# Kernel optimization log

Hardware: AMD Instinct MI355X
Metric: run time of the kernel (lower is better)

## Reference

```python
import jax, jax.numpy as jnp
import numpy as np

EPS = 1e-5

def _ln(x, g, b):
    mu = jnp.mean(x, -1, keepdims=True)
    var = jnp.mean((x - mu) ** 2, -1, keepdims=True)
    return (x - mu) / jnp.sqrt(var + EPS) * g + b

def _edge_scores(x, lat, mask, sn_g, sn_b, tn_g, tn_b, su_w, su_b, tp_w, tp_b, m1_w, m1_b, m2_w, m2_b):
    # x: [B,S,D], lat: [B,K,D] -> edges [B,S,K]
    s = _ln(x, sn_g, sn_b) @ su_w + su_b      # [B,S,E]
    t = _ln(lat, tn_g, tn_b) @ tp_w + tp_b    # [B,K,E]
    B, S, E = s.shape
    K = t.shape[1]
    s4 = jnp.broadcast_to(s[:, :, None, :], (B, S, K, E))
    t4 = jnp.broadcast_to(t[:, None, :, :], (B, S, K, E))
    pair = jnp.concatenate([s4, t4, s4 * t4], axis=-1)  # [B,S,K,3E]
    h = jax.nn.gelu(pair @ m1_w + m1_b, approximate=False)
    e = (h @ m2_w + m2_b)[..., 0]             # [B,S,K]
    e = e / (1.0 + jnp.abs(e))                # softsign
    return e * mask[:, :, None]

def setup_inputs() -> dict:
    key = jax.random.key(0)
    B, St, Si, K, D, E = 2, 2048, 1024, 64, 768, 256
    ks = iter(jax.random.split(key, 64))
    d = {}
    d['text_values'] = jax.random.normal(next(ks), (B, St, D), jnp.float32)
    d['image_values'] = jax.random.normal(next(ks), (B, Si, D), jnp.float32)
    d['latent_state_init'] = jax.random.normal(next(ks), (B, K, D), jnp.float32)
    d['latent_value_init'] = jax.random.normal(next(ks), (B, K, D), jnp.float32)
    d['text_mask'] = jnp.ones((B, St), jnp.float32)
    d['image_mask'] = jnp.ones((B, Si), jnp.float32)
    def scorer(prefix):
        d[prefix + 'sn_g'] = jnp.ones((D,), jnp.float32)
        d[prefix + 'sn_b'] = jnp.zeros((D,), jnp.float32)
        d[prefix + 'tn_g'] = jnp.ones((D,), jnp.float32)
        d[prefix + 'tn_b'] = jnp.zeros((D,), jnp.float32)
        d[prefix + 'su_w'] = jax.random.normal(next(ks), (D, E), jnp.float32) * 0.02
        d[prefix + 'su_b'] = jnp.zeros((E,), jnp.float32)
        d[prefix + 'tp_w'] = jax.random.normal(next(ks), (D, E), jnp.float32) * 0.02
        d[prefix + 'tp_b'] = jnp.zeros((E,), jnp.float32)
        d[prefix + 'm1_w'] = jax.random.normal(next(ks), (3 * E, E), jnp.float32) * 0.02
        d[prefix + 'm1_b'] = jnp.zeros((E,), jnp.float32)
        d[prefix + 'm2_w'] = jax.random.normal(next(ks), (E, 1), jnp.float32) * 0.02
        d[prefix + 'm2_b'] = jnp.zeros((1,), jnp.float32)
    scorer('t_')
    scorer('i_')
    for p in ['tsn', 'isn', 'stn', 'vn']:
        d[p + '_g'] = jnp.ones((D,), jnp.float32)
        d[p + '_b'] = jnp.zeros((D,), jnp.float32)
    d['tsp_w'] = jax.random.normal(next(ks), (D, D), jnp.float32) * 0.02
    d['tsp_b'] = jnp.zeros((D,), jnp.float32)
    d['isp_w'] = jax.random.normal(next(ks), (D, D), jnp.float32) * 0.02
    d['isp_b'] = jnp.zeros((D,), jnp.float32)
    return d

def reference(text_values, image_values, latent_state_init, latent_value_init, text_mask, image_mask,
              t_sn_g, t_sn_b, t_tn_g, t_tn_b, t_su_w, t_su_b, t_tp_w, t_tp_b, t_m1_w, t_m1_b, t_m2_w, t_m2_b,
              i_sn_g, i_sn_b, i_tn_g, i_tn_b, i_su_w, i_su_b, i_tp_w, i_tp_b, i_m1_w, i_m1_b, i_m2_w, i_m2_b,
              tsn_g, tsn_b, isn_g, isn_b, stn_g, stn_b, vn_g, vn_b, tsp_w, tsp_b, isp_w, isp_b):
    t2l = _edge_scores(text_values, latent_value_init, text_mask,
                       t_sn_g, t_sn_b, t_tn_g, t_tn_b, t_su_w, t_su_b, t_tp_w, t_tp_b, t_m1_w, t_m1_b, t_m2_w, t_m2_b)
    i2l = _edge_scores(image_values, latent_value_init, image_mask,
                       i_sn_g, i_sn_b, i_tn_g, i_tn_b, i_su_w, i_su_b, i_tp_w, i_tp_b, i_m1_w, i_m1_b, i_m2_w, i_m2_b)
    tsf = _ln(text_values, tsn_g, tsn_b) @ tsp_w + tsp_b    # [B,St,D]
    isf = _ln(image_values, isn_g, isn_b) @ isp_w + isp_b   # [B,Si,D]
    state_raw = jnp.einsum('bsk,bsd->bkd', t2l, tsf) + jnp.einsum('bsk,bsd->bkd', i2l, isf)
    value_raw = jnp.einsum('bsk,bsd->bkd', t2l, text_values) + jnp.einsum('bsk,bsd->bkd', i2l, image_values)
    latent_state = _ln(state_raw + latent_state_init, stn_g, stn_b)
    latent_value = _ln(value_raw + latent_value_init, vn_g, vn_b)
    return latent_state, latent_value, t2l, i2l
```

## Files before the change

kernel.cpp:

```cpp
#include <hip/hip_runtime.h>
#include <math.h>

#define EPS_LN 1e-5f

#define B_  2
#define ST_ 2048
#define SI_ 1024
#define K_  64
#define D_  768
#define E_  256

typedef __bf16 bf16x8 __attribute__((ext_vector_type(8)));
typedef float  f32x4  __attribute__((ext_vector_type(4)));
typedef unsigned short ushort_t;

__device__ inline ushort_t f2bf(float x) {
    unsigned int u = __float_as_uint(x);
    unsigned int r = (u + 0x7FFFu + ((u >> 16) & 1u)) >> 16;
    return (ushort_t)r;
}

__device__ inline float gelu_fast(float z) {
    float a = fabsf(z);
    float t = __expf(a * -1.702f);
    float r = __builtin_amdgcn_rcpf(1.0f + t);
    float th = fmaf(t * r, -2.0f, 1.0f);
    return fmaf(0.5f * a, th, 0.5f * z);
}


__device__ void ln_stats_body(int bid, int tid,
    const float* __restrict__ xt, const float* __restrict__ xi,
    const float* __restrict__ xl, float* __restrict__ mu, float* __restrict__ rstd)
{
    int w = tid >> 6, lane = tid & 63;
    int row = bid * 4 + w;
    const float* src;
    if (row < 4096) src = xt + (size_t)row * D_;
    else if (row < 6144) src = xi + (size_t)(row - 4096) * D_;
    else src = xl + (size_t)(row - 6144) * D_;
    float s = 0.f, q = 0.f;
    #pragma unroll
    for (int rep = 0; rep < 3; ++rep) {
        float4 v = *(const float4*)(src + lane * 4 + rep * 256);
        s += v.x + v.y + v.z + v.w;
        q += v.x * v.x + v.y * v.y + v.z * v.z + v.w * v.w;
    }
    #pragma unroll
    for (int off = 32; off > 0; off >>= 1) {
        s += __shfl_xor(s, off, 64);
        q += __shfl_xor(q, off, 64);
    }
    if (lane == 0) {
        float m = s / (float)D_;
        float var = q / (float)D_ - m * m;
        mu[row] = m;
        rstd[row] = rsqrtf(var + EPS_LN);
    }
}

__device__ void sgemm_body(char* smem, int tid,
    const float* __restrict__ A, const float* __restrict__ Bm,
    const float* __restrict__ rowScale, const float* __restrict__ bias,
    const float* __restrict__ muA, const float* __restrict__ sdA, int so,
    float* __restrict__ C, int kz, int bx, int by, int Kd, int N)
{
    float (*As)[65] = (float(*)[65])smem;
    float (*Bs)[64] = (float(*)[64])(smem + 16 * 65 * 4);
    int tx = tid & 15, ty = tid >> 4;
    int row0 = by * 64;
    int col0 = bx * 64;
    float acc[4][4] = {};
    int kbase = kz * 128;
    for (int k0 = kbase; k0 < kbase + 128; k0 += 16) {
        {
            int e = tid * 4;
            int r = e >> 4, kk = e & 15;
            float4 av = *(const float4*)(A + (size_t)(row0 + r) * Kd + k0 + kk);
            if (muA) {
                float m = muA[so + row0 + r], sd = sdA[so + row0 + r];
                av.x = (av.x - m) * sd; av.y = (av.y - m) * sd;
                av.z = (av.z - m) * sd; av.w = (av.w - m) * sd;
            }
            As[kk + 0][r] = av.x; As[kk + 1][r] = av.y; As[kk + 2][r] = av.z; As[kk + 3][r] = av.w;
        }
        {
            int e = tid * 4;
            int kk = e >> 6, c = e & 63;
            float4 bv = *(const float4*)(Bm + (size_t)(k0 + kk) * N + col0 + c);
            if (rowScale) {
                float sc = rowScale[k0 + kk];
                bv.x *= sc; bv.y *= sc; bv.z *= sc; bv.w *= sc;
            }
            *(float4*)&Bs[kk][c] = bv;
        }
        __syncthreads();
        #pragma unroll
        for (int kk = 0; kk < 16; ++kk) {
            float a[4], b[4];
            #pragma unroll
            for (int i = 0; i < 4; ++i) a[i] = As[kk][ty + 16 * i];
            #pragma unroll
            for (int j = 0; j < 4; ++j) b[j] = Bs[kk][tx + 16 * j];
            #pragma unroll
            for (int i = 0; i < 4; ++i)
                #pragma unroll
                for (int j = 0; j < 4; ++j)
                    acc[i][j] += a[i] * b[j];
        }
        __syncthreads();
    }
    #pragma unroll
    for (int i = 0; i < 4; ++i) {
        int r = row0 + ty + 16 * i;
        #pragma unroll
        for (int j = 0; j < 4; ++j) {
            int c = col0 + tx + 16 * j;
            float v = acc[i][j];
            if (kz == 0 && bias) v += bias[c];
            atomicAdd(&C[(size_t)r * N + c], v);
        }
    }
}

__global__ __launch_bounds__(256) void prelude_kernel(
    const float* __restrict__ xt, const float* __restrict__ xi,
    const float* __restrict__ xl, float* __restrict__ mu, float* __restrict__ rstd,
    const float* b0, const float* W0, const float* w0, float* f0,
    const float* b1, const float* W1, const float* w1, float* f1,
    const float* b2, const float* W2, const float* w2, float* f2,
    const float* b3, const float* W3, const float* w3, float* f3,
    const float* b4, const float* W4, const float* w4, float* f4,
    const float* b5, const float* W5, const float* w5, float* f5,
    const float* __restrict__ Wsu_t, const float* __restrict__ g_t, ushort_t* __restrict__ WF_t,
    const float* __restrict__ Wsu_i, const float* __restrict__ g_i, ushort_t* __restrict__ WF_i)
{
    extern __shared__ __align__(16) char smem[];
    int bid = blockIdx.x;
    int tid = threadIdx.x;
    if (bid < 1568) {
        ln_stats_body(bid, tid, xt, xi, xl, mu, rstd);
        return;
    }
    if (bid < 2432) {
        int f = bid - 1568;
        int ebx = f % 12, dby = (f / 12) % 12, cfg = f / 144;
        const float* blns[6] = {b0, b1, b2, b3, b4, b5};
        const float* Ws[6]   = {W0, W1, W2, W3, W4, W5};
        const float* wbs[6]  = {w0, w1, w2, w3, w4, w5};
        float* bfs[6]        = {f0, f1, f2, f3, f4, f5};
        int E = (cfg >= 4) ? 768 : 256;
        if (ebx * 64 >= E) return;
        const float* bln = blns[cfg];
        const float* W = Ws[cfg];
        float (*red)[64] = (float(*)[64])smem;
        int c = tid & 63, part = tid >> 6;
        int e = ebx * 64 + c;
        int d0 = dby * 64;
        float s = 0.f;
        #pragma unroll
        for (int i = 0; i < 16; ++i) {
            int d = d0 + part * 16 + i;
            s += bln[d] * W[(size_t)d * E + e];
        }
        red[part][c] = s; __syncthreads();
        if (part == 0) {
            float v = red[0][c] + red[1][c] + red[2][c] + red[3][c];
            if (dby == 0 && wbs[cfg]) v += wbs[cfg][e];
            atomicAdd(&bfs[cfg][e], v);
        }
        return;
    }
    {
        const int HALF = (D_ >> 5) * (E_ >> 4) * 64;
        int gidx = (bid - 2432) * 256 + tid;
        int isImg = gidx >= HALF;
        int idx = isImg ? gidx - HALF : gidx;
        const float* W = isImg ? Wsu_i : Wsu_t;
        const float* g = isImg ? g_i : g_t;
        ushort_t* out = isImg ? WF_i : WF_t;
        int lane = idx & 63;
        int ntile = (idx >> 6) & 15;
        int c = idx >> 10;
        int n = ntile * 16 + (lane & 15);
        int k0 = c * 32 + (lane >> 4) * 8;
        ushort_t o[8];
        #pragma unroll
        for (int j = 0; j < 8; ++j) {
            int k = k0 + j;
            o[j] = f2bf(W[(size_t)k * E_ + n] * g[k]);
        }
        *reinterpret_cast<uint4*>(out + (size_t)idx * 8) = *reinterpret_cast<uint4*>(o);
    }
}

__global__ __launch_bounds__(256) void stage2_kernel(
    const float* __restrict__ xt, const float* __restrict__ xi,
    const float* __restrict__ mu, const float* __restrict__ rstd,
    ushort_t* __restrict__ XrF_t, ushort_t* __restrict__ XhF_t, ushort_t* __restrict__ AF_t,
    ushort_t* __restrict__ XrF_i, ushort_t* __restrict__ XhF_i, ushort_t* __restrict__ AF_i,
    const float* __restrict__ lat,
    const float* __restrict__ t_tp_w, const float* __restrict__ t_tn_g,
    const float* __restrict__ b_tp_t, float* __restrict__ t_t,
    const float* __restrict__ i_tp_w, const float* __restrict__ i_tn_g,
    const float* __restrict__ b_tp_i, float* __restrict__ t_i)
{
    extern __shared__ __align__(16) char smem[];
    int bid = blockIdx.x;
    int t = threadIdx.x;
    if (bid < 1152) {
        int bx = bid % 96, by = bid / 96;
        float (*tile)[65] = (float(*)[65])smem;
        float* mu_s = (float*)(smem + 64 * 65 * 4);
        float* rs_s = mu_s + 64;
        int isImg = bx >= 64;
        const float* x = isImg ? xi : xt;
        ushort_t* XrF = isImg ? XrF_i : XrF_t;
        ushort_t* XhF = isImg ? XhF_i : XhF_t;
        ushort_t* AF  = isImg ? AF_i  : AF_t;
        int rbase = (isImg ? bx - 64 : bx) * 64;
        int statOff = isImg ? 4096 : 0;
        int d0 = by * 64;
        #pragma unroll
        for (int rep = 0; rep < 4; ++rep) {
            int rl = (t >> 4) + rep * 16;
            int c4 = (t & 15) * 4;
            *(float4*)&tile[rl][c4] = *(const float4*)(x + (size_t)(rbase + rl) * D_ + d0 + c4);
        }
        if (t < 64) { mu_s[t] = mu[statOff + rbase + t]; rs_s[t] = rstd[statOff + rbase + t]; }
        __syncthreads();
        int lane = t & 63;
        #pragma unroll
        for (int rep = 0; rep < 2; ++rep) {
            int idx = t + rep * 256;
            int nt = (idx >> 6) & 3, cl = (idx >> 8) & 1;
            int kl = cl * 32 + (lane >> 4) * 8;
            int nl = nt * 16 + (lane & 15);
            ushort_t orw[8], oh[8];
            #pragma unroll
            for (int j = 0; j < 8; ++j) {
                float v = tile[kl + j][nl];
                orw[j] = f2bf(v);
                oh[j]  = f2bf((v - mu_s[kl + j]) * rs_s[kl + j]);
            }
            size_t chunk = (size_t)((rbase >> 5) + cl);
            size_t o = ((chunk * 48 + (d0 >> 4) + nt) * 64 + lane) * 8;
            *reinterpret_cast<uint4*>(XrF + o) = *reinterpret_cast<uint4*>(orw);
            *reinterpret_cast<uint4*>(XhF + o) = *reinterpret_cast<uint4*>(oh);
        }
        #pragma unroll
        for (int rep = 0; rep < 2; ++rep) {
            int idx = t + rep * 256;
            int cl = (idx >> 6) & 1, tl = idx >> 7;
            int rl = tl * 16 + (lane & 15);
            int dl = cl * 32 + (lane >> 4) * 8;
            float m = mu_s[rl], rs = rs_s[rl];
            ushort_t o8[8];
            #pragma unroll
            for (int j = 0; j < 8; ++j)
                o8[j] = f2bf((tile[rl][dl + j] - m) * rs);
            size_t o = (((size_t)(rbase >> 4) + tl) * 24 + (d0 >> 5) + cl) * 512 + lane * 8;
            *reinterpret_cast<uint4*>(AF + o) = *reinterpret_cast<uint4*>(o8);
        }
        return;
    }
    {
        int f = bid - 1152;
        int bx = f % 4, by = (f / 4) % 2, z = f / 8;
        int cfg = (z >= 6) ? 1 : 0;
        int kz = cfg ? z - 6 : z;
        sgemm_body(smem, t,
                   lat, cfg ? i_tp_w : t_tp_w, cfg ? i_tn_g : t_tn_g,
                   cfg ? b_tp_i : b_tp_t, mu, rstd, 6144,
                   cfg ? t_i : t_t, kz, bx, by, D_, E_);
    }
}

__global__ __launch_bounds__(256) void stage3_kernel(
    const float* __restrict__ t_t, const float* __restrict__ t_i,
    const float* __restrict__ t_m1_w, const float* __restrict__ t_m1_b,
    const float* __restrict__ i_m1_w, const float* __restrict__ i_m1_b,
    float* __restrict__ c2_t, float* __restrict__ c2_i,
    const ushort_t* __restrict__ AF_t, const ushort_t* __restrict__ BF_t,
    const float* __restrict__ b_su_t, ushort_t* __restrict__ sF_t,
    const ushort_t* __restrict__ AF_i, const ushort_t* __restrict__ BF_i,
    const float* __restrict__ b_su_i, ushort_t* __restrict__ sF_i,
    ushort_t* __restrict__ MF_t, ushort_t* __restrict__ MF_i)
{
    extern __shared__ __align__(16) char smem[];
    int bid = blockIdx.x;
    int tid = threadIdx.x;
    if (bid < 32) {
        int bx = bid % 4, by = (bid / 4) % 2, z = bid / 8;
        int cfg = (z >= 2) ? 1 : 0;
        int kz = cfg ? z - 2 : z;
        sgemm_body(smem, tid,
                   cfg ? t_i : t_t,
                   (cfg ? i_m1_w : t_m1_w) + (size_t)E_ * E_, nullptr,
                   cfg ? i_m1_b : t_m1_b, nullptr, nullptr, 0,
                   cfg ? c2_i : c2_t, kz, bx, by, E_, E_);
        return;
    }
    if (bid < 224) {
        int bx = bid - 32;
        int isImg = bx >= 128;
        const ushort_t* AF = isImg ? AF_i : AF_t;
        const ushort_t* BF = isImg ? BF_i : BF_t;
        const float* bias = isImg ? b_su_i : b_su_t;
        ushort_t* sF = isImg ? sF_i : sF_t;
        int tile0 = (isImg ? bx - 128 : bx) * 2;
        ushort_t* lsbase = (ushort_t*)smem;
        int w = tid >> 6, lane = tid & 63;
        int quad = lane >> 4, n16 = lane & 15;
        f32x4 acc[2][4];
        #pragma unroll
        for (int mt = 0; mt < 2; ++mt)
            #pragma unroll
            for (int nt = 0; nt < 4; ++nt)
                acc[mt][nt] = (f32x4){0.f, 0.f, 0.f, 0.f};
        for (int c = 0; c < 24; ++c) {
            bf16x8 af[2], bf[4];
            #pragma unroll
            for (int mt = 0; mt < 2; ++mt)
                af[mt] = *reinterpret_cast<const bf16x8*>(AF + ((size_t)(tile0 + mt) * 24 + c) * 512 + lane * 8);
            #pragma unroll
            for (int nt = 0; nt < 4; ++nt)
                bf[nt] = *reinterpret_cast<const bf16x8*>(BF + ((size_t)c * 16 + w * 4 + nt) * 512 + lane * 8);
            #pragma unroll
            for (int mt = 0; mt < 2; ++mt)
                #pragma unroll
                for (int nt = 0; nt < 4; ++nt)
                    acc[mt][nt] = __builtin_amdgcn_mfma_f32_16x16x32_bf16(af[mt], bf[nt], acc[mt][nt], 0, 0, 0);
        }
        #pragma unroll
        for (int mt = 0; mt < 2; ++mt)
            #pragma unroll
            for (int nt = 0; nt < 4; ++nt) {
                float bv = bias[w * 64 + nt * 16 + n16];
                #pragma unroll
                for (int r = 0; r < 4; ++r)
                    lsbase[(w * 32 + mt * 16 + quad * 4 + r) * 72 + nt * 16 + n16] = f2bf(acc[mt][nt][r] + bv);
            }
        __syncthreads();
        #pragma unroll
        for (int mt = 0; mt < 2; ++mt)
            #pragma unroll
            for (int h = 0; h < 2; ++h) {
                uint4 v = *reinterpret_cast<const uint4*>(&lsbase[(w * 32 + mt * 16 + n16) * 72 + h * 32 + quad * 8]);
                *reinterpret_cast<uint4*>(sF + ((size_t)(tile0 + mt) * 8 + 2 * w + h) * 512 + lane * 8) = v;
            }
        return;
    }
    {
        const int HALF = B_ * K_ * 16 * 8 * 64;
        int gidx = (bid - 224) * 256 + tid;
        int isImg = gidx >= HALF;
        int idx = isImg ? gidx - HALF : gidx;
        const float* tP = isImg ? t_i : t_t;
        const float* W3 = (isImg ? i_m1_w : t_m1_w) + 2 * (size_t)E_ * E_;
        const float* W1 = isImg ? i_m1_w : t_m1_w;
        ushort_t* MF = isImg ? MF_i : MF_t;
        int lane = idx & 63;
        int kc = (idx >> 6) & 7;
        int nt = (idx >> 9) & 15;
        int bk = idx >> 13;
        int n = nt * 16 + (lane & 15);
        int e0 = kc * 32 + (lane >> 4) * 8;
        ushort_t out[8];
        #pragma unroll
        for (int j = 0; j < 8; ++j) {
            int e = e0 + j;
            float v = tP[(size_t)bk * E_ + e] * W3[(size_t)e * E_ + n] + W1[(size_t)e * E_ + n];
            out[j] = f2bf(v);
        }
        *reinterpret_cast<uint4*>(MF + (size_t)idx * 8) = *reinterpret_cast<uint4*>(out);
    }
}

__global__ __launch_bounds__(256, 4) void cross_mfma_kernel(
    const ushort_t* __restrict__ sF_t, const ushort_t* __restrict__ MF_t,
    const float* __restrict__ c2_t, const float* __restrict__ m2w_t,
    const float* __restrict__ m2b_t, const float* __restrict__ mask_t,
    float* __restrict__ Et,
    const ushort_t* __restrict__ sF_i, const ushort_t* __restrict__ MF_i,
    const float* __restrict__ c2_i, const float* __restrict__ m2w_i,
    const float* __restrict__ m2b_i, const float* __restrict__ mask_i,
    float* __restrict__ Ei)
{
    int k = blockIdx.x;
    int by = blockIdx.y;
    int isImg = by >= 32;
    int S = isImg ? SI_ : ST_;
    const ushort_t* sF = isImg ? sF_i : sF_t;
    const ushort_t* MF = isImg ? MF_i : MF_t;
    const float* c2P = isImg ? c2_i : c2_t;
    const float* m2w = isImg ? m2w_i : m2w_t;
    const float* m2b = isImg ? m2b_i : m2b_t;
    const float* mask = isImg ? mask_i : mask_t;
    float* Etmp = isImg ? Ei : Et;
    int s0 = (isImg ? by - 32 : by) * 64;
    int b = blockIdx.z;
    int tid = threadIdx.x;
    int w = tid >> 6, lane = tid & 63;
    int quad = lane >> 4, n16 = lane & 15;

    const ushort_t* aBase = sF + (size_t)(b * (S / 16) + (s0 >> 4)) * 4096;
    const ushort_t* bBase = MF + ((size_t)(b * K_ + k) * 16 + w * 4) * 4096;

    f32x4 acc[4][4];
    #pragma unroll
    for (int mt = 0; mt < 4; ++mt)
        #pragma unroll
        for (int nt = 0; nt < 4; ++nt)
            acc[mt][nt] = (f32x4){0.f, 0.f, 0.f, 0.f};

    #pragma unroll
    for (int kc = 0; kc < 8; ++kc) {
        bf16x8 bfr[4], af[4];
        #pragma unroll
        for (int nt = 0; nt < 4; ++nt)
            bfr[nt] = *reinterpret_cast<const bf16x8*>(bBase + (size_t)nt * 4096 + kc * 512 + lane * 8);
        #pragma unroll
        for (int mt = 0; mt < 4; ++mt)
            af[mt] = *reinterpret_cast<const bf16x8*>(aBase + (size_t)mt * 4096 + kc * 512 + lane * 8);
        #pragma unroll
        for (int mt = 0; mt < 4; ++mt)
            #pragma unroll
            for (int nt = 0; nt < 4; ++nt)
                acc[mt][nt] = __builtin_amdgcn_mfma_f32_16x16x32_bf16(af[mt], bfr[nt], acc[mt][nt], 0, 0, 0);
    }

    const float* c2v = c2P + (size_t)(b * K_ + k) * E_;
    float c2r[4], m2r[4];
    #pragma unroll
    for (int nt = 0; nt < 4; ++nt) {
        int col = w * 64 + nt * 16 + n16;
        c2r[nt] = c2v[col];
        m2r[nt] = m2w[col];
    }
    __shared__ float pPart[4][64];
    #pragma unroll
    for (int mt = 0; mt < 4; ++mt) {
        #pragma unroll
        for (int r = 0; r < 4; ++r) {
            float p = 0.f;
            #pragma unroll
            for (int nt = 0; nt < 4; ++nt) {
                float z = acc[mt][nt][r] + c2r[nt];
                p += gelu_fast(z) * m2r[nt];
            }
            p += __shfl_xor(p, 1, 64);
            p += __shfl_xor(p, 2, 64);
            p += __shfl_xor(p, 4, 64);
            p += __shfl_xor(p, 8, 64);
            if (n16 == 0) pPart[w][mt * 16 + quad * 4 + r] = p;
        }
    }
    __syncthreads();
    if (tid < 64) {
        float e = pPart[0][tid] + pPart[1][tid] + pPart[2][tid] + pPart[3][tid] + m2b[0];
        e = e / (1.0f + fabsf(e));
        int srow = s0 + tid;
        e *= mask[(size_t)b * S + srow];
        Etmp[(size_t)(b * K_ + k) * S + srow] = e;
    }
}

__global__ __launch_bounds__(256) void packE2_kernel(
    const float* __restrict__ Et, const float* __restrict__ Ei,
    float* __restrict__ t2l, float* __restrict__ i2l,
    ushort_t* __restrict__ EF_t, ushort_t* __restrict__ EF_i,
    float* __restrict__ rs_t, float* __restrict__ rs_i)
{
    __shared__ float tile[64][33];
    int g = blockIdx.x;
    int isImg = g >= 128;
    const float* Esrc = isImg ? Ei : Et;
    float* dst = isImg ? i2l : t2l;
    ushort_t* EF = isImg ? EF_i : EF_t;
    float* rsum = isImg ? rs_i : rs_t;
    int chunk = isImg ? g - 128 : g;
    int S = isImg ? SI_ : ST_;
    int b = (chunk * 32) / S;
    int s0 = (chunk * 32) % S;
    int t = threadIdx.x;
    {
        int k = t >> 2, si = (t & 3) * 8;
        const float* p = Esrc + (size_t)(b * K_ + k) * S + s0 + si;
        *(float4*)&tile[k][si] = *(const float4*)p;
        *(float4*)&tile[k][si + 4] = *(const float4*)(p + 4);
    }
    __syncthreads();
    {
        int s = t >> 3, k0 = (t & 7) * 8;
        float o[8];
        #pragma unroll
        for (int j = 0; j < 8; ++j) o[j] = tile[k0 + j][s];
        float* p = dst + ((size_t)b * S + s0 + s) * K_ + k0;
        *(float4*)p = *(float4*)&o[0];
        *(float4*)(p + 4) = *(float4*)&o[4];
    }
    {
        int mt = t >> 6, lane = t & 63;
        int k = mt * 16 + (lane & 15);
        int sl0 = (lane >> 4) * 8;
        ushort_t o8[8];
        #pragma unroll
        for (int j = 0; j < 8; ++j)
            o8[j] = f2bf(tile[k][sl0 + j]);
        *reinterpret_cast<uint4*>(EF + (((size_t)chunk * 4 + mt) * 64 + lane) * 8) = *reinterpret_cast<uint4*>(o8);
    }
    if (t < 64) {
        float s = 0.f;
        #pragma unroll
        for (int j = 0; j < 32; ++j) s += tile[t][j];
        atomicAdd(&rsum[b * K_ + t], s);
    }
}

__global__ __launch_bounds__(256, 4) void einsum_mfma_kernel(
    const ushort_t* __restrict__ EF_t, const ushort_t* __restrict__ XhF_t,
    const ushort_t* __restrict__ XrF_t, float* __restrict__ PtG, float* __restrict__ PtR,
    const ushort_t* __restrict__ EF_i, const ushort_t* __restrict__ XhF_i,
    const ushort_t* __restrict__ XrF_i, float* __restrict__ PiG, float* __restrict__ PiR)
{
    int bz = blockIdx.z;
    int isImg = bz >= 2;
    int b = isImg ? bz - 2 : bz;
    int S = isImg ? SI_ : ST_;
    const ushort_t* EF = isImg ? EF_i : EF_t;
    const ushort_t* XhF = isImg ? XhF_i : XhF_t;
    const ushort_t* XrF = isImg ? XrF_i : XrF_t;
    float* PG = isImg ? PiG : PtG;
    float* PR = isImg ? PiR : PtR;
    int chunksPerBlock = isImg ? 2 : 4;

    int w = threadIdx.x >> 6, lane = threadIdx.x & 63;
    int quad = lane >> 4, n16 = lane & 15;
    int y = blockIdx.y;
    int nt0 = blockIdx.x * 8 + w * 2;
    size_t cb = (size_t)(b * S) / 32 + (size_t)y * chunksPerBlock;

    f32x4 aG[4][2], aR[4][2];
    #pragma unroll
    for (int mt = 0; mt < 4; ++mt)
        #pragma unroll
        for (int nt = 0; nt < 2; ++nt) {
            aG[mt][nt] = (f32x4){0.f, 0.f, 0.f, 0.f};
            aR[mt][nt] = (f32x4){0.f, 0.f, 0.f, 0.f};
        }

    for (int cc = 0; cc < chunksPerBlock; ++cc) {
        size_t c = cb + cc;
        bf16x8 af[4], bh[2], bx[2];
        #pragma unroll
        for (int mt = 0; mt < 4; ++mt)
            af[mt] = *reinterpret_cast<const bf16x8*>(EF + ((c * 4 + mt) * 64 + lane) * 8);
        #pragma unroll
        for (int nt = 0; nt < 2; ++nt) {
            bh[nt] = *reinterpret_cast<const bf16x8*>(XhF + ((c * 48 + nt0 + nt) * 64 + lane) * 8);
            bx[nt] = *reinterpret_cast<const bf16x8*>(XrF + ((c * 48 + nt0 + nt) * 64 + lane) * 8);
        }
        #pragma unroll
        for (int mt = 0; mt < 4; ++mt)
            #pragma unroll
            for (int nt = 0; nt < 2; ++nt) {
                aG[mt][nt] = __builtin_amdgcn_mfma_f32_16x16x32_bf16(af[mt], bh[nt], aG[mt][nt], 0, 0, 0);
                aR[mt][nt] = __builtin_amdgcn_mfma_f32_16x16x32_bf16(af[mt], bx[nt], aR[mt][nt], 0, 0, 0);
            }
    }
    #pragma unroll
    for (int mt = 0; mt < 4; ++mt)
        #pragma unroll
        for (int nt = 0; nt < 2; ++nt) {
            int d = (nt0 + nt) * 16 + n16;
            #pragma unroll
            for (int r = 0; r < 4; ++r) {
                int krow = mt * 16 + quad * 4 + r;
                size_t o = (((size_t)y * B_ + b) * K_ + krow) * D_ + d;
                PG[o] = aG[mt][nt][r];
                PR[o] = aR[mt][nt][r];
            }
        }
}

__global__ __launch_bounds__(256) void reduce_parts_kernel(
    const float* __restrict__ PtG, const float* __restrict__ PtR,
    const float* __restrict__ PiG, const float* __restrict__ PiR,
    float* __restrict__ Gt, float* __restrict__ Gi, float* __restrict__ Racc)
{
    const int BKD = B_ * K_ * D_;
    int idx = blockIdx.x * 256 + threadIdx.x;
    if (idx >= BKD) return;
    float gt = 0.f, gi = 0.f, r = 0.f;
    #pragma unroll
    for (int c = 0; c < 16; ++c) { gt += PtG[(size_t)c * BKD + idx]; r += PtR[(size_t)c * BKD + idx]; }
    #pragma unroll
    for (int c = 0; c < 16; ++c) { gi += PiG[(size_t)c * BKD + idx]; r += PiR[(size_t)c * BKD + idx]; }
    Gt[idx] = gt; Gi[idx] = gi; Racc[idx] = r;
}

__global__ __launch_bounds__(256) void sgemm3_kernel(
    const float* __restrict__ Gt, const float* __restrict__ tsp_w, const float* __restrict__ tsn_g,
    const float* __restrict__ Gi, const float* __restrict__ isp_w, const float* __restrict__ isn_g,
    float* __restrict__ state_tmp)
{
    extern __shared__ __align__(16) char smem[];
    int f = blockIdx.x;
    int bx = f % 12, by = (f / 12) % 2, z = f / 24;
    int cfg = (z >= 6) ? 1 : 0;
    int kz = cfg ? z - 6 : z;
    sgemm_body(smem, threadIdx.x,
               cfg ? Gi : Gt, cfg ? isp_w : tsp_w, cfg ? isn_g : tsn_g,
               nullptr, nullptr, nullptr, 0, state_tmp, kz, bx, by, D_, D_);
}

__global__ __launch_bounds__(256) void final_ln_kernel(
    const float* __restrict__ stateTmp, const float* __restrict__ Racc,
    const float* __restrict__ rs_t, const float* __restrict__ rs_i,
    const float* __restrict__ b_tspf, const float* __restrict__ b_ispf,
    const float* __restrict__ state_init, const float* __restrict__ value_init,
    const float* __restrict__ stn_g, const float* __restrict__ stn_b,
    const float* __restrict__ vn_g, const float* __restrict__ vn_b,
    float* __restrict__ outState, float* __restrict__ outValue)
{
    __shared__ float pre[D_];
    __shared__ float red[256];
    int idx = blockIdx.x;
    int row = idx & 127;
    int isVal = idx >> 7;
    int tid = threadIdx.x;
    if (!isVal) {
        float rt = rs_t[row], ri = rs_i[row];
        for (int d = tid; d < D_; d += 256)
            pre[d] = stateTmp[(size_t)row * D_ + d] + rt * b_tspf[d] + ri * b_ispf[d]
                   + state_init[(size_t)row * D_ + d];
    } else {
        for (int d = tid; d < D_; d += 256)
            pre[d] = Racc[(size_t)row * D_ + d] + value_init[(size_t)row * D_ + d];
    }
    __syncthreads();
    float s = 0.f;
    for (int d = tid; d < D_; d += 256) s += pre[d];
    red[tid] = s; __syncthreads();
    for (int off = 128; off > 0; off >>= 1) { if (tid < off) red[tid] += red[tid + off]; __syncthreads(); }
    float mu = red[0] / (float)D_;
    __syncthreads();
    float v = 0.f;
    for (int d = tid; d < D_; d += 256) { float t = pre[d] - mu; v += t * t; }
    red[tid] = v; __syncthreads();
    for (int off = 128; off > 0; off >>= 1) { if (tid < off) red[tid] += red[tid + off]; __syncthreads(); }
    float rstd = rsqrtf(red[0] / (float)D_ + EPS_LN);
    const float* g  = isVal ? vn_g : stn_g;
    const float* bb = isVal ? vn_b : stn_b;
    float* o = (isVal ? outValue : outState) + (size_t)row * D_;
    for (int d = tid; d < D_; d += 256) o[d] = (pre[d] - mu) * rstd * g[d] + bb[d];
}

extern "C" void kernel_launch(void* const* d_in, const int* in_sizes, int n_in,
                              void* d_out, int out_size, void* d_ws, size_t ws_size,
                              hipStream_t stream) {
    const float* text_values  = (const float*)d_in[0];
    const float* image_values = (const float*)d_in[1];
    const float* lstate_init  = (const float*)d_in[2];
    const float* lvalue_init  = (const float*)d_in[3];
    const float* text_mask    = (const float*)d_in[4];
    const float* image_mask   = (const float*)d_in[5];
    const float* t_sn_g = (const float*)d_in[6];
    const float* t_sn_b = (const float*)d_in[7];
    const float* t_tn_g = (const float*)d_in[8];
    const float* t_tn_b = (const float*)d_in[9];
    const float* t_su_w = (const float*)d_in[10];
    const float* t_su_b = (const float*)d_in[11];
    const float* t_tp_w = (const float*)d_in[12];
    const float* t_tp_b = (const float*)d_in[13];
    const float* t_m1_w = (const float*)d_in[14];
    const float* t_m1_b = (const float*)d_in[15];
    const float* t_m2_w = (const float*)d_in[16];
    const float* t_m2_b = (const float*)d_in[17];
    const float* i_sn_g = (const float*)d_in[18];
    const float* i_sn_b = (const float*)d_in[19];
    const float* i_tn_g = (const float*)d_in[20];
    const float* i_tn_b = (const float*)d_in[21];
    const float* i_su_w = (const float*)d_in[22];
    const float* i_su_b = (const float*)d_in[23];
    const float* i_tp_w = (const float*)d_in[24];
    const float* i_tp_b = (const float*)d_in[25];
    const float* i_m1_w = (const float*)d_in[26];
    const float* i_m1_b = (const float*)d_in[27];
    const float* i_m2_w = (const float*)d_in[28];
    const float* i_m2_b = (const float*)d_in[29];
    const float* tsn_g = (const float*)d_in[30];
    const float* tsn_b = (const float*)d_in[31];
    const float* isn_g = (const float*)d_in[32];
    const float* isn_b = (const float*)d_in[33];
    const float* stn_g = (const float*)d_in[34];
    const float* stn_b = (const float*)d_in[35];
    const float* vn_g  = (const float*)d_in[36];
    const float* vn_b  = (const float*)d_in[37];
    const float* tsp_w = (const float*)d_in[38];
    const float* tsp_b = (const float*)d_in[39];
    const float* isp_w = (const float*)d_in[40];
    const float* isp_b = (const float*)d_in[41];

    float* ws = (float*)d_ws;
    size_t o = 0;
    float* stats_mu = ws + o; o += 6272;
    float* stats_rs = ws + o; o += 6272;
    float* zeroBase = ws + o;
    float* b_su_t = ws + o; o += E_;
    float* b_su_i = ws + o; o += E_;
    float* b_tp_t = ws + o; o += E_;
    float* b_tp_i = ws + o; o += E_;
    float* b_tspf = ws + o; o += D_;
    float* b_ispf = ws + o; o += D_;
    float* t_t  = ws + o; o += (size_t)B_ * K_ * E_;
    float* t_i  = ws + o; o += (size_t)B_ * K_ * E_;
    float* c2_t = ws + o; o += (size_t)B_ * K_ * E_;
    float* c2_i = ws + o; o += (size_t)B_ * K_ * E_;
    float* state_tmp = ws + o; o += (size_t)B_ * K_ * D_;
    float* rs_t = ws + o; o += 128;
    float* rs_i = ws + o; o += 128;
    size_t zeroFloats = (size_t)(4 * E_ + 2 * D_ + 4 * B_ * K_ * E_ + B_ * K_ * D_ + 256);
    float* Etmp_t = ws + o; o += (size_t)B_ * K_ * ST_;
    float* Etmp_i = ws + o; o += (size_t)B_ * K_ * SI_;
    ushort_t* AF_t = (ushort_t*)(ws + o); o += (size_t)B_ * ST_ * D_ / 2;
    ushort_t* AF_i = (ushort_t*)(ws + o); o += (size_t)B_ * SI_ * D_ / 2;
    ushort_t* WsuF_t = (ushort_t*)(ws + o); o += (size_t)D_ * E_ / 2;
    ushort_t* WsuF_i = (ushort_t*)(ws + o); o += (size_t)D_ * E_ / 2;
    ushort_t* sF_t = (ushort_t*)(ws + o); o += (size_t)B_ * ST_ * E_ / 2;
    ushort_t* sF_i = (ushort_t*)(ws + o); o += (size_t)B_ * SI_ * E_ / 2;
    ushort_t* MF_t = (ushort_t*)(ws + o); o += (size_t)B_ * K_ * E_ * E_ / 2;
    ushort_t* MF_i = (ushort_t*)(ws + o); o += (size_t)B_ * K_ * E_ * E_ / 2;
    ushort_t* XhF_t = (ushort_t*)(ws + o); o += (size_t)B_ * ST_ * D_ / 2;
    ushort_t* XhF_i = (ushort_t*)(ws + o); o += (size_t)B_ * SI_ * D_ / 2;
    ushort_t* XrF_t = (ushort_t*)(ws + o); o += (size_t)B_ * ST_ * D_ / 2;
    ushort_t* XrF_i = (ushort_t*)(ws + o); o += (size_t)B_ * SI_ * D_ / 2;
    ushort_t* EF_t  = (ushort_t*)(ws + o); o += (size_t)B_ * ST_ * K_ / 2;
    ushort_t* EF_i  = (ushort_t*)(ws + o); o += (size_t)B_ * SI_ * K_ / 2;
    const int BKD = B_ * K_ * D_;
    float* PtG = ws + o; o += (size_t)16 * BKD;
    float* PtR = ws + o; o += (size_t)16 * BKD;
    float* PiG = ws + o; o += (size_t)16 * BKD;
    float* PiR = ws + o; o += (size_t)16 * BKD;
    float* Gt   = ws + o; o += BKD;
    float* Gi   = ws + o; o += BKD;
    float* Racc = ws + o; o += BKD;

    float* outState = (float*)d_out;
    float* outValue = (float*)d_out + (size_t)B_ * K_ * D_;
    float* t2l = (float*)d_out + 2 * (size_t)B_ * K_ * D_;
    float* i2l = t2l + (size_t)B_ * ST_ * K_;

    hipMemsetAsync(zeroBase, 0, zeroFloats * sizeof(float), stream);

    prelude_kernel<<<2624, 256, 1024, stream>>>(
        text_values, image_values, lvalue_init, stats_mu, stats_rs,
        t_sn_b, t_su_w, t_su_b, b_su_t,
        i_sn_b, i_su_w, i_su_b, b_su_i,
        t_tn_b, t_tp_w, t_tp_b, b_tp_t,
        i_tn_b, i_tp_w, i_tp_b, b_tp_i,
        tsn_b, tsp_w, tsp_b, b_tspf,
        isn_b, isp_w, isp_b, b_ispf,
        t_su_w, t_sn_g, WsuF_t,
        i_su_w, i_sn_g, WsuF_i);

    stage2_kernel<<<1248, 256, 17152, stream>>>(
        text_values, image_values, stats_mu, stats_rs,
        XrF_t, XhF_t, AF_t, XrF_i, XhF_i, AF_i,
        lvalue_init,
        t_tp_w, t_tn_g, b_tp_t, t_t,
        i_tp_w, i_tn_g, b_tp_i, t_i);

    stage3_kernel<<<8416, 256, 18432, stream>>>(
        t_t, t_i, t_m1_w, t_m1_b, i_m1_w, i_m1_b, c2_t, c2_i,
        AF_t, WsuF_t, b_su_t, sF_t,
        AF_i, WsuF_i, b_su_i, sF_i,
        MF_t, MF_i);

    cross_mfma_kernel<<<dim3(K_, 48, B_), 256, 0, stream>>>(
        sF_t, MF_t, c2_t, t_m2_w, t_m2_b, text_mask, Etmp_t,
        sF_i, MF_i, c2_i, i_m2_w, i_m2_b, image_mask, Etmp_i);

    packE2_kernel<<<192, 256, 0, stream>>>(
        Etmp_t, Etmp_i, t2l, i2l, EF_t, EF_i, rs_t, rs_i);

    einsum_mfma_kernel<<<dim3(6, 16, 4), 256, 0, stream>>>(
        EF_t, XhF_t, XrF_t, PtG, PtR,
        EF_i, XhF_i, XrF_i, PiG, PiR);

    reduce_parts_kernel<<<(BKD + 255) / 256, 256, 0, stream>>>(PtG, PtR, PiG, PiR, Gt, Gi, Racc);

    sgemm3_kernel<<<288, 256, 8256, stream>>>(
        Gt, tsp_w, tsn_g, Gi, isp_w, isn_g, state_tmp);

    final_ln_kernel<<<2 * B_ * K_, 256, 0, stream>>>(
        state_tmp, Racc, rs_t, rs_i, b_tspf, b_ispf,
        lstate_init, lvalue_init, stn_g, stn_b, vn_g, vn_b, outState, outValue);
}
```

Before: 329.2 us.

## Merge pipeline stages, fuse LN into su GEMM, fold E packing into einsum

Reduces the launch chain by removing the memset, the separate stage2/stage3 split and the packE2 kernel. The latent projection and bias-fold GEMMs move into the prelude and run over the full K range with direct stores instead of split-K atomics. The s GEMM now normalises raw x to bf16 on the fly rather than reading a pre-packed AF buffer. The einsum converts fp32 edge scores to bf16 inline and also writes the transposed t2l/i2l outputs and row sums. The cost is serial-K work in a few blocks and more redundant global reads of x and E.

```diff
diff --git a/kernel.cpp b/kernel.cpp
--- a/kernel.cpp
+++ b/kernel.cpp
@@ -28,51 +28,17 @@
     return fmaf(0.5f * a, th, 0.5f * z);
 }
 
-
-__device__ void ln_stats_body(int bid, int tid,
-    const float* __restrict__ xt, const float* __restrict__ xi,
-    const float* __restrict__ xl, float* __restrict__ mu, float* __restrict__ rstd)
-{
-    int w = tid >> 6, lane = tid & 63;
-    int row = bid * 4 + w;
-    const float* src;
-    if (row < 4096) src = xt + (size_t)row * D_;
-    else if (row < 6144) src = xi + (size_t)(row - 4096) * D_;
-    else src = xl + (size_t)(row - 6144) * D_;
-    float s = 0.f, q = 0.f;
-    #pragma unroll
-    for (int rep = 0; rep < 3; ++rep) {
-        float4 v = *(const float4*)(src + lane * 4 + rep * 256);
-        s += v.x + v.y + v.z + v.w;
-        q += v.x * v.x + v.y * v.y + v.z * v.z + v.w * v.w;
-    }
-    #pragma unroll
-    for (int off = 32; off > 0; off >>= 1) {
-        s += __shfl_xor(s, off, 64);
-        q += __shfl_xor(q, off, 64);
-    }
-    if (lane == 0) {
-        float m = s / (float)D_;
-        float var = q / (float)D_ - m * m;
-        mu[row] = m;
-        rstd[row] = rsqrtf(var + EPS_LN);
-    }
-}
-
-__device__ void sgemm_body(char* smem, int tid,
-    const float* __restrict__ A, const float* __restrict__ Bm,
-    const float* __restrict__ rowScale, const float* __restrict__ bias,
-    const float* __restrict__ muA, const float* __restrict__ sdA, int so,
-    float* __restrict__ C, int kz, int bx, int by, int Kd, int N)
+__device__ void sgemm_acc_body(char* smem, int tid,
+    const float* A, const float* Bm, const float* rowScale,
+    const float* muA, const float* sdA, int so,
+    float acc[4][4], int bx, int by, int k0beg, int k0end, int Kd, int N)
 {
     float (*As)[65] = (float(*)[65])smem;
     float (*Bs)[64] = (float(*)[64])(smem + 16 * 65 * 4);
     int tx = tid & 15, ty = tid >> 4;
     int row0 = by * 64;
     int col0 = bx * 64;
-    float acc[4][4] = {};
-    int kbase = kz * 128;
-    for (int k0 = kbase; k0 < kbase + 128; k0 += 16) {
+    for (int k0 = k0beg; k0 < k0end; k0 += 16) {
         {
             int e = tid * 4;
             int r = e >> 4, kk = e & 15;
@@ -110,22 +76,12 @@
         }
         __syncthreads();
     }
-    #pragma unroll
-    for (int i = 0; i < 4; ++i) {
-        int r = row0 + ty + 16 * i;
-        #pragma unroll
-        for (int j = 0; j < 4; ++j) {
-            int c = col0 + tx + 16 * j;
-            float v = acc[i][j];
-            if (kz == 0 && bias) v += bias[c];
-            atomicAdd(&C[(size_t)r * N + c], v);
-        }
-    }
 }
 
 __global__ __launch_bounds__(256) void prelude_kernel(
     const float* __restrict__ xt, const float* __restrict__ xi,
-    const float* __restrict__ xl, float* __restrict__ mu, float* __restrict__ rstd,
+    const float* __restrict__ lat,
+    float* __restrict__ mu, float* __restrict__ rstd,
     const float* b0, const float* W0, const float* w0, float* f0,
     const float* b1, const float* W1, const float* w1, float* f1,
     const float* b2, const float* W2, const float* w2, float* f2,
@@ -133,47 +89,85 @@
     const float* b4, const float* W4, const float* w4, float* f4,
     const float* b5, const float* W5, const float* w5, float* f5,
     const float* __restrict__ Wsu_t, const float* __restrict__ g_t, ushort_t* __restrict__ WF_t,
-    const float* __restrict__ Wsu_i, const float* __restrict__ g_i, ushort_t* __restrict__ WF_i)
+    const float* __restrict__ Wsu_i, const float* __restrict__ g_i, ushort_t* __restrict__ WF_i,
+    const float* __restrict__ t_tp_w, const float* __restrict__ t_tn_g,
+    const float* __restrict__ b_tp_t, float* __restrict__ t_t,
+    const float* __restrict__ i_tp_w, const float* __restrict__ i_tn_g,
+    const float* __restrict__ b_tp_i, float* __restrict__ t_i,
+    float* __restrict__ rs_t, float* __restrict__ rs_i)
 {
     extern __shared__ __align__(16) char smem[];
     int bid = blockIdx.x;
     int tid = threadIdx.x;
-    if (bid < 1568) {
-        ln_stats_body(bid, tid, xt, xi, xl, mu, rstd);
+    if (bid < 16) {
+        int bx = bid & 3, by = (bid >> 2) & 1, cfg = bid >> 3;
+        float* smu = (float*)(smem + 8256);
+        float* srs = smu + 64;
+        int row0 = by * 64;
+        {
+            int r = tid >> 2, part = tid & 3;
+            const float* xr = lat + (size_t)(row0 + r) * D_ + part * 192;
+            float s = 0.f, q = 0.f;
+            for (int i = 0; i < 192; i += 4) {
+                float4 v = *(const float4*)(xr + i);
+                s += v.x + v.y + v.z + v.w;
+                q += v.x * v.x + v.y * v.y + v.z * v.z + v.w * v.w;
+            }
+            s += __shfl_xor(s, 1, 64); q += __shfl_xor(q, 1, 64);
+            s += __shfl_xor(s, 2, 64); q += __shfl_xor(q, 2, 64);
+            if (part == 0) {
+                float m = s / (float)D_;
+                smu[r] = m;
+                srs[r] = rsqrtf(q / (float)D_ - m * m + EPS_LN);
+            }
+        }
+        __syncthreads();
+        float acc[4][4] = {};
+        sgemm_acc_body(smem, tid, lat, cfg ? i_tp_w : t_tp_w, cfg ? i_tn_g : t_tn_g,
+                       smu, srs, -row0, acc, bx, by, 0, D_, D_, E_);
+        const float* bias = cfg ? b_tp_i : b_tp_t;
+        float* C = cfg ? t_i : t_t;
+        int tx = tid & 15, ty = tid >> 4;
+        #pragma unroll
+        for (int i = 0; i < 4; ++i) {
+            int r = row0 + ty + 16 * i;
+            #pragma unroll
+            for (int j = 0; j < 4; ++j) {
+                int c = bx * 64 + tx + 16 * j;
+                C[(size_t)r * E_ + c] = acc[i][j] + bias[c];
+            }
+        }
         return;
     }
-    if (bid < 2432) {
-        int f = bid - 1568;
-        int ebx = f % 12, dby = (f / 12) % 12, cfg = f / 144;
+    if (bid < 56) {
+        int f = bid - 16;
+        int cfg, ebx;
+        if (f < 16) { cfg = f >> 2; ebx = f & 3; }
+        else { f -= 16; cfg = 4 + f / 12; ebx = f % 12; }
         const float* blns[6] = {b0, b1, b2, b3, b4, b5};
         const float* Ws[6]   = {W0, W1, W2, W3, W4, W5};
         const float* wbs[6]  = {w0, w1, w2, w3, w4, w5};
         float* bfs[6]        = {f0, f1, f2, f3, f4, f5};
         int E = (cfg >= 4) ? 768 : 256;
-        if (ebx * 64 >= E) return;
         const float* bln = blns[cfg];
         const float* W = Ws[cfg];
         float (*red)[64] = (float(*)[64])smem;
         int c = tid & 63, part = tid >> 6;
         int e = ebx * 64 + c;
-        int d0 = dby * 64;
         float s = 0.f;
-        #pragma unroll
-        for (int i = 0; i < 16; ++i) {
-            int d = d0 + part * 16 + i;
+        for (int d = part * 192; d < part * 192 + 192; ++d)
             s += bln[d] * W[(size_t)d * E + e];
-        }
         red[part][c] = s; __syncthreads();
         if (part == 0) {
             float v = red[0][c] + red[1][c] + red[2][c] + red[3][c];
-            if (dby == 0 && wbs[cfg]) v += wbs[cfg][e];
-            atomicAdd(&bfs[cfg][e], v);
+            if (wbs[cfg]) v += wbs[cfg][e];
+            bfs[cfg][e] = v;
         }
         return;
     }
-    {
+    if (bid < 248) {
         const int HALF = (D_ >> 5) * (E_ >> 4) * 64;
-        int gidx = (bid - 2432) * 256 + tid;
+        int gidx = (bid - 56) * 256 + tid;
         int isImg = gidx >= HALF;
         int idx = isImg ? gidx - HALF : gidx;
         const float* W = isImg ? Wsu_i : Wsu_t;
@@ -191,25 +185,144 @@
             o[j] = f2bf(W[(size_t)k * E_ + n] * g[k]);
         }
         *reinterpret_cast<uint4*>(out + (size_t)idx * 8) = *reinterpret_cast<uint4*>(o);
-    }
-}
-
-__global__ __launch_bounds__(256) void stage2_kernel(
+        return;
+    }
+    if (bid < 1784) {
+        int rb = bid - 248;
+        int w = tid >> 6, lane = tid & 63;
+        int row = rb * 4 + w;
+        const float* src = (row < 4096) ? xt + (size_t)row * D_
+                                        : xi + (size_t)(row - 4096) * D_;
+        float s = 0.f, q = 0.f;
+        #pragma unroll
+        for (int rep = 0; rep < 3; ++rep) {
+            float4 v = *(const float4*)(src + lane * 4 + rep * 256);
+            s += v.x + v.y + v.z + v.w;
+            q += v.x * v.x + v.y * v.y + v.z * v.z + v.w * v.w;
+        }
+        #pragma unroll
+        for (int off = 32; off > 0; off >>= 1) {
+            s += __shfl_xor(s, off, 64);
+            q += __shfl_xor(q, off, 64);
+        }
+        if (lane == 0) {
+            float m = s / (float)D_;
+            mu[row] = m;
+            rstd[row] = rsqrtf(q / (float)D_ - m * m + EPS_LN);
+        }
+        return;
+    }
+    if (tid < 128) rs_t[tid] = 0.f;
+    else rs_i[tid - 128] = 0.f;
+}
+
+__global__ __launch_bounds__(256) void bigpack_kernel(
+    const float* __restrict__ t_t, const float* __restrict__ t_i,
+    const float* __restrict__ t_m1_w, const float* __restrict__ t_m1_b,
+    const float* __restrict__ i_m1_w, const float* __restrict__ i_m1_b,
+    float* __restrict__ c2_t, float* __restrict__ c2_i,
     const float* __restrict__ xt, const float* __restrict__ xi,
     const float* __restrict__ mu, const float* __restrict__ rstd,
-    ushort_t* __restrict__ XrF_t, ushort_t* __restrict__ XhF_t, ushort_t* __restrict__ AF_t,
-    ushort_t* __restrict__ XrF_i, ushort_t* __restrict__ XhF_i, ushort_t* __restrict__ AF_i,
-    const float* __restrict__ lat,
-    const float* __restrict__ t_tp_w, const float* __restrict__ t_tn_g,
-    const float* __restrict__ b_tp_t, float* __restrict__ t_t,
-    const float* __restrict__ i_tp_w, const float* __restrict__ i_tn_g,
-    const float* __restrict__ b_tp_i, float* __restrict__ t_i)
+    const ushort_t* __restrict__ WF_t, const float* __restrict__ b_su_t, ushort_t* __restrict__ sF_t,
+    const ushort_t* __restrict__ WF_i, const float* __restrict__ b_su_i, ushort_t* __restrict__ sF_i,
+    ushort_t* __restrict__ XrF_t, ushort_t* __restrict__ XhF_t,
+    ushort_t* __restrict__ XrF_i, ushort_t* __restrict__ XhF_i,
+    ushort_t* __restrict__ MF_t, ushort_t* __restrict__ MF_i)
 {
     extern __shared__ __align__(16) char smem[];
     int bid = blockIdx.x;
-    int t = threadIdx.x;
-    if (bid < 1152) {
-        int bx = bid % 96, by = bid / 96;
+    int tid = threadIdx.x;
+    if (bid < 16) {
+        int bx = bid & 3, by = (bid >> 2) & 1, cfg = bid >> 3;
+        float acc[4][4] = {};
+        sgemm_acc_body(smem, tid, cfg ? t_i : t_t,
+                       (cfg ? i_m1_w : t_m1_w) + (size_t)E_ * E_, nullptr,
+                       nullptr, nullptr, 0, acc, bx, by, 0, E_, E_, E_);
+        const float* bias = cfg ? i_m1_b : t_m1_b;
+        float* C = cfg ? c2_i : c2_t;
+        int tx = tid & 15, ty = tid >> 4;
+        #pragma unroll
+        for (int i = 0; i < 4; ++i) {
+            int r = by * 64 + ty + 16 * i;
+            #pragma unroll
+            for (int j = 0; j < 4; ++j) {
+                int c = bx * 64 + tx + 16 * j;
+                C[(size_t)r * E_ + c] = acc[i][j] + bias[c];
+            }
+        }
+        return;
+    }
+    if (bid < 208) {
+        int bx = bid - 16;
+        int isImg = bx >= 128;
+        const float* xsrc = isImg ? xi : xt;
+        const ushort_t* BF = isImg ? WF_i : WF_t;
+        const float* bias = isImg ? b_su_i : b_su_t;
+        ushort_t* sF = isImg ? sF_i : sF_t;
+        const float* muP = mu + (isImg ? 4096 : 0);
+        const float* rsP = rstd + (isImg ? 4096 : 0);
+        int tile0 = (isImg ? bx - 128 : bx) * 2;
+        ushort_t* lsbase = (ushort_t*)smem;
+        int w = tid >> 6, lane = tid & 63;
+        int quad = lane >> 4, n16 = lane & 15;
+        int row[2]; float rmu[2], rrs[2];
+        #pragma unroll
+        for (int mt = 0; mt < 2; ++mt) {
+            row[mt] = (tile0 + mt) * 16 + n16;
+            rmu[mt] = muP[row[mt]];
+            rrs[mt] = rsP[row[mt]];
+        }
+        f32x4 acc[2][4];
+        #pragma unroll
+        for (int mt = 0; mt < 2; ++mt)
+            #pragma unroll
+            for (int nt = 0; nt < 4; ++nt)
+                acc[mt][nt] = (f32x4){0.f, 0.f, 0.f, 0.f};
+        for (int c = 0; c < 24; ++c) {
+            bf16x8 af[2], bf[4];
+            #pragma unroll
+            for (int mt = 0; mt < 2; ++mt) {
+                const float* p = xsrc + (size_t)row[mt] * D_ + c * 32 + quad * 8;
+                float4 a = *(const float4*)p;
+                float4 b = *(const float4*)(p + 4);
+                ushort_t o8[8] = {
+                    f2bf((a.x - rmu[mt]) * rrs[mt]), f2bf((a.y - rmu[mt]) * rrs[mt]),
+                    f2bf((a.z - rmu[mt]) * rrs[mt]), f2bf((a.w - rmu[mt]) * rrs[mt]),
+                    f2bf((b.x - rmu[mt]) * rrs[mt]), f2bf((b.y - rmu[mt]) * rrs[mt]),
+                    f2bf((b.z - rmu[mt]) * rrs[mt]), f2bf((b.w - rmu[mt]) * rrs[mt]) };
+                af[mt] = *reinterpret_cast<bf16x8*>(o8);
+            }
+            #pragma unroll
+            for (int nt = 0; nt < 4; ++nt)
+                bf[nt] = *reinterpret_cast<const bf16x8*>(BF + ((size_t)c * 16 + w * 4 + nt) * 512 + lane * 8);
+            #pragma unroll
+            for (int mt = 0; mt < 2; ++mt)
+                #pragma unroll
+                for (int nt = 0; nt < 4; ++nt)
+                    acc[mt][nt] = __builtin_amdgcn_mfma_f32_16x16x32_bf16(af[mt], bf[nt], acc[mt][nt], 0, 0, 0);
+        }
+        #pragma unroll
+        for (int mt = 0; mt < 2; ++mt)
+            #pragma unroll
+            for (int nt = 0; nt < 4; ++nt) {
+                float bv = bias[w * 64 + nt * 16 + n16];
+                #pragma unroll
+                for (int r = 0; r < 4; ++r)
+                    lsbase[(w * 32 + mt * 16 + quad * 4 + r) * 72 + nt * 16 + n16] = f2bf(acc[mt][nt][r] + bv);
+            }
+        __syncthreads();
+        #pragma unroll
+        for (int mt = 0; mt < 2; ++mt)
+            #pragma unroll
+            for (int h = 0; h < 2; ++h) {
+                uint4 v = *reinterpret_cast<const uint4*>(&lsbase[(w * 32 + mt * 16 + n16) * 72 + h * 32 + quad * 8]);
+                *reinterpret_cast<uint4*>(sF + ((size_t)(tile0 + mt) * 8 + 2 * w + h) * 512 + lane * 8) = v;
+            }
+        return;
+    }
+    if (bid < 1360) {
+        int f = bid - 208;
+        int bx = f % 96, by = f / 96;
         float (*tile)[65] = (float(*)[65])smem;
         float* mu_s = (float*)(smem + 64 * 65 * 4);
         float* rs_s = mu_s + 64;
@@ -217,10 +330,10 @@
         const float* x = isImg ? xi : xt;
         ushort_t* XrF = isImg ? XrF_i : XrF_t;
         ushort_t* XhF = isImg ? XhF_i : XhF_t;
-        ushort_t* AF  = isImg ? AF_i  : AF_t;
         int rbase = (isImg ? bx - 64 : bx) * 64;
         int statOff = isImg ? 4096 : 0;
         int d0 = by * 64;
+        int t = tid;
         #pragma unroll
         for (int rep = 0; rep < 4; ++rep) {
             int rl = (t >> 4) + rep * 16;
@@ -248,112 +361,11 @@
             *reinterpret_cast<uint4*>(XrF + o) = *reinterpret_cast<uint4*>(orw);
             *reinterpret_cast<uint4*>(XhF + o) = *reinterpret_cast<uint4*>(oh);
         }
-        #pragma unroll
-        for (int rep = 0; rep < 2; ++rep) {
-            int idx = t + rep * 256;
-            int cl = (idx >> 6) & 1, tl = idx >> 7;
-            int rl = tl * 16 + (lane & 15);
-            int dl = cl * 32 + (lane >> 4) * 8;
-            float m = mu_s[rl], rs = rs_s[rl];
-            ushort_t o8[8];
-            #pragma unroll
-            for (int j = 0; j < 8; ++j)
-                o8[j] = f2bf((tile[rl][dl + j] - m) * rs);
-            size_t o = (((size_t)(rbase >> 4) + tl) * 24 + (d0 >> 5) + cl) * 512 + lane * 8;
-            *reinterpret_cast<uint4*>(AF + o) = *reinterpret_cast<uint4*>(o8);
-        }
-        return;
-    }
-    {
-        int f = bid - 1152;
-        int bx = f % 4, by = (f / 4) % 2, z = f / 8;
-        int cfg = (z >= 6) ? 1 : 0;
-        int kz = cfg ? z - 6 : z;
-        sgemm_body(smem, t,
-                   lat, cfg ? i_tp_w : t_tp_w, cfg ? i_tn_g : t_tn_g,
-                   cfg ? b_tp_i : b_tp_t, mu, rstd, 6144,
-                   cfg ? t_i : t_t, kz, bx, by, D_, E_);
-    }
-}
-
-__global__ __launch_bounds__(256) void stage3_kernel(
-    const float* __restrict__ t_t, const float* __restrict__ t_i,
-    const float* __restrict__ t_m1_w, const float* __restrict__ t_m1_b,
-    const float* __restrict__ i_m1_w, const float* __restrict__ i_m1_b,
-    float* __restrict__ c2_t, float* __restrict__ c2_i,
-    const ushort_t* __restrict__ AF_t, const ushort_t* __restrict__ BF_t,
-    const float* __restrict__ b_su_t, ushort_t* __restrict__ sF_t,
-    const ushort_t* __restrict__ AF_i, const ushort_t* __restrict__ BF_i,
-    const float* __restrict__ b_su_i, ushort_t* __restrict__ sF_i,
-    ushort_t* __restrict__ MF_t, ushort_t* __restrict__ MF_i)
-{
-    extern __shared__ __align__(16) char smem[];
-    int bid = blockIdx.x;
-    int tid = threadIdx.x;
-    if (bid < 32) {
-        int bx = bid % 4, by = (bid / 4) % 2, z = bid / 8;
-        int cfg = (z >= 2) ? 1 : 0;
-        int kz = cfg ? z - 2 : z;
-        sgemm_body(smem, tid,
-                   cfg ? t_i : t_t,
-                   (cfg ? i_m1_w : t_m1_w) + (size_t)E_ * E_, nullptr,
-                   cfg ? i_m1_b : t_m1_b, nullptr, nullptr, 0,
-                   cfg ? c2_i : c2_t, kz, bx, by, E_, E_);
-        return;
-    }
-    if (bid < 224) {
-        int bx = bid - 32;
-        int isImg = bx >= 128;
-        const ushort_t* AF = isImg ? AF_i : AF_t;
-        const ushort_t* BF = isImg ? BF_i : BF_t;
-        const float* bias = isImg ? b_su_i : b_su_t;
-        ushort_t* sF = isImg ? sF_i : sF_t;
-        int tile0 = (isImg ? bx - 128 : bx) * 2;
-        ushort_t* lsbase = (ushort_t*)smem;
-        int w = tid >> 6, lane = tid & 63;
-        int quad = lane >> 4, n16 = lane & 15;
-        f32x4 acc[2][4];
-        #pragma unroll
-        for (int mt = 0; mt < 2; ++mt)
-            #pragma unroll
-            for (int nt = 0; nt < 4; ++nt)
-                acc[mt][nt] = (f32x4){0.f, 0.f, 0.f, 0.f};
-        for (int c = 0; c < 24; ++c) {
-            bf16x8 af[2], bf[4];
-            #pragma unroll
-            for (int mt = 0; mt < 2; ++mt)
-                af[mt] = *reinterpret_cast<const bf16x8*>(AF + ((size_t)(tile0 + mt) * 24 + c) * 512 + lane * 8);
-            #pragma unroll
-            for (int nt = 0; nt < 4; ++nt)
-                bf[nt] = *reinterpret_cast<const bf16x8*>(BF + ((size_t)c * 16 + w * 4 + nt) * 512 + lane * 8);
-            #pragma unroll
-            for (int mt = 0; mt < 2; ++mt)
-                #pragma unroll
-                for (int nt = 0; nt < 4; ++nt)
-                    acc[mt][nt] = __builtin_amdgcn_mfma_f32_16x16x32_bf16(af[mt], bf[nt], acc[mt][nt], 0, 0, 0);
-        }
-        #pragma unroll
-        for (int mt = 0; mt < 2; ++mt)
-            #pragma unroll
-            for (int nt = 0; nt < 4; ++nt) {
-                float bv = bias[w * 64 + nt * 16 + n16];
-                #pragma unroll
-                for (int r = 0; r < 4; ++r)
-                    lsbase[(w * 32 + mt * 16 + quad * 4 + r) * 72 + nt * 16 + n16] = f2bf(acc[mt][nt][r] + bv);
-            }
-        __syncthreads();
-        #pragma unroll
-        for (int mt = 0; mt < 2; ++mt)
-            #pragma unroll
-            for (int h = 0; h < 2; ++h) {
-                uint4 v = *reinterpret_cast<const uint4*>(&lsbase[(w * 32 + mt * 16 + n16) * 72 + h * 32 + quad * 8]);
-                *reinterpret_cast<uint4*>(sF + ((size_t)(tile0 + mt) * 8 + 2 * w + h) * 512 + lane * 8) = v;
-            }
         return;
     }
     {
         const int HALF = B_ * K_ * 16 * 8 * 64;
-        int gidx = (bid - 224) * 256 + tid;
+        int gidx = (bid - 1360) * 256 + tid;
         int isImg = gidx >= HALF;
         int idx = isImg ? gidx - HALF : gidx;
         const float* tP = isImg ? t_i : t_t;
@@ -466,69 +478,20 @@
     }
 }
 
-__global__ __launch_bounds__(256) void packE2_kernel(
-    const float* __restrict__ Et, const float* __restrict__ Ei,
+__global__ __launch_bounds__(256, 4) void einsum_mfma_kernel(
+    const float* __restrict__ Et, const ushort_t* __restrict__ XhF_t,
+    const ushort_t* __restrict__ XrF_t, float* __restrict__ PtG, float* __restrict__ PtR,
+    const float* __restrict__ Ei, const ushort_t* __restrict__ XhF_i,
+    const ushort_t* __restrict__ XrF_i, float* __restrict__ PiG, float* __restrict__ PiR,
     float* __restrict__ t2l, float* __restrict__ i2l,
-    ushort_t* __restrict__ EF_t, ushort_t* __restrict__ EF_i,
     float* __restrict__ rs_t, float* __restrict__ rs_i)
 {
     __shared__ float tile[64][33];
-    int g = blockIdx.x;
-    int isImg = g >= 128;
-    const float* Esrc = isImg ? Ei : Et;
-    float* dst = isImg ? i2l : t2l;
-    ushort_t* EF = isImg ? EF_i : EF_t;
-    float* rsum = isImg ? rs_i : rs_t;
-    int chunk = isImg ? g - 128 : g;
-    int S = isImg ? SI_ : ST_;
-    int b = (chunk * 32) / S;
-    int s0 = (chunk * 32) % S;
-    int t = threadIdx.x;
-    {
-        int k = t >> 2, si = (t & 3) * 8;
-        const float* p = Esrc + (size_t)(b * K_ + k) * S + s0 + si;
-        *(float4*)&tile[k][si] = *(const float4*)p;
-        *(float4*)&tile[k][si + 4] = *(const float4*)(p + 4);
-    }
-    __syncthreads();
-    {
-        int s = t >> 3, k0 = (t & 7) * 8;
-        float o[8];
-        #pragma unroll
-        for (int j = 0; j < 8; ++j) o[j] = tile[k0 + j][s];
-        float* p = dst + ((size_t)b * S + s0 + s) * K_ + k0;
-        *(float4*)p = *(float4*)&o[0];
-        *(float4*)(p + 4) = *(float4*)&o[4];
-    }
-    {
-        int mt = t >> 6, lane = t & 63;
-        int k = mt * 16 + (lane & 15);
-        int sl0 = (lane >> 4) * 8;
-        ushort_t o8[8];
-        #pragma unroll
-        for (int j = 0; j < 8; ++j)
-            o8[j] = f2bf(tile[k][sl0 + j]);
-        *reinterpret_cast<uint4*>(EF + (((size_t)chunk * 4 + mt) * 64 + lane) * 8) = *reinterpret_cast<uint4*>(o8);
-    }
-    if (t < 64) {
-        float s = 0.f;
-        #pragma unroll
-        for (int j = 0; j < 32; ++j) s += tile[t][j];
-        atomicAdd(&rsum[b * K_ + t], s);
-    }
-}
-
-__global__ __launch_bounds__(256, 4) void einsum_mfma_kernel(
-    const ushort_t* __restrict__ EF_t, const ushort_t* __restrict__ XhF_t,
-    const ushort_t* __restrict__ XrF_t, float* __restrict__ PtG, float* __restrict__ PtR,
-    const ushort_t* __restrict__ EF_i, const ushort_t* __restrict__ XhF_i,
-    const ushort_t* __restrict__ XrF_i, float* __restrict__ PiG, float* __restrict__ PiR)
-{
     int bz = blockIdx.z;
     int isImg = bz >= 2;
     int b = isImg ? bz - 2 : bz;
     int S = isImg ? SI_ : ST_;
-    const ushort_t* EF = isImg ? EF_i : EF_t;
+    const float* Esrc = isImg ? Ei : Et;
     const ushort_t* XhF = isImg ? XhF_i : XhF_t;
     const ushort_t* XrF = isImg ? XrF_i : XrF_t;
     float* PG = isImg ? PiG : PtG;
@@ -552,10 +515,18 @@
 
     for (int cc = 0; cc < chunksPerBlock; ++cc) {
         size_t c = cb + cc;
+        int s0 = (y * chunksPerBlock + cc) * 32;
         bf16x8 af[4], bh[2], bx[2];
         #pragma unroll
-        for (int mt = 0; mt < 4; ++mt)
-            af[mt] = *reinterpret_cast<const bf16x8*>(EF + ((c * 4 + mt) * 64 + lane) * 8);
+        for (int mt = 0; mt < 4; ++mt) {
+            int kk = mt * 16 + n16;
+            const float* p = Esrc + (size_t)(b * K_ + kk) * S + s0 + quad * 8;
+            float4 a = *(const float4*)p;
+            float4 bb4 = *(const float4*)(p + 4);
+            ushort_t o8[8] = { f2bf(a.x), f2bf(a.y), f2bf(a.z), f2bf(a.w),
+                               f2bf(bb4.x), f2bf(bb4.y), f2bf(bb4.z), f2bf(bb4.w) };
+            af[mt] = *reinterpret_cast<bf16x8*>(o8);
+        }
         #pragma unroll
         for (int nt = 0; nt < 2; ++nt) {
             bh[nt] = *reinterpret_cast<const bf16x8*>(XhF + ((c * 48 + nt0 + nt) * 64 + lane) * 8);
@@ -582,12 +553,45 @@
                 PR[o] = aR[mt][nt][r];
             }
         }
+
+    if (blockIdx.x == 0) {
+        float* dst = isImg ? i2l : t2l;
+        float* rsum = isImg ? rs_i : rs_t;
+        int t = threadIdx.x;
+        float ksum = 0.f;
+        for (int cc = 0; cc < chunksPerBlock; ++cc) {
+            int s0 = (y * chunksPerBlock + cc) * 32;
+            {
+                int kk = t >> 2, si = (t & 3) * 8;
+                const float* p = Esrc + (size_t)(b * K_ + kk) * S + s0 + si;
+                *(float4*)&tile[kk][si] = *(const float4*)p;
+                *(float4*)&tile[kk][si + 4] = *(const float4*)(p + 4);
+            }
+            __syncthreads();
+            {
+                int s = t >> 3, k0 = (t & 7) * 8;
+                float o[8];
+                #pragma unroll
+                for (int j = 0; j < 8; ++j) o[j] = tile[k0 + j][s];
+                float* p = dst + ((size_t)b * S + s0 + s) * K_ + k0;
+                *(float4*)p = *(float4*)&o[0];
+                *(float4*)(p + 4) = *(float4*)&o[4];
+            }
+            if (t < 64) {
+                #pragma unroll
+                for (int j = 0; j < 32; ++j) ksum += tile[t][j];
+            }
+            __syncthreads();
+        }
+        if (t < 64) atomicAdd(&rsum[b * K_ + t], ksum);
+    }
 }
 
 __global__ __launch_bounds__(256) void reduce_parts_kernel(
     const float* __restrict__ PtG, const float* __restrict__ PtR,
     const float* __restrict__ PiG, const float* __restrict__ PiR,
-    float* __restrict__ Gt, float* __restrict__ Gi, float* __restrict__ Racc)
+    float* __restrict__ Gt, float* __restrict__ Gi, float* __restrict__ Racc,
+    float* __restrict__ state_tmp)
 {
     const int BKD = B_ * K_ * D_;
     int idx = blockIdx.x * 256 + threadIdx.x;
@@ -598,6 +602,7 @@
     #pragma unroll
     for (int c = 0; c < 16; ++c) { gi += PiG[(size_t)c * BKD + idx]; r += PiR[(size_t)c * BKD + idx]; }
     Gt[idx] = gt; Gi[idx] = gi; Racc[idx] = r;
+    state_tmp[idx] = 0.f;
 }
 
 __global__ __launch_bounds__(256) void sgemm3_kernel(
@@ -610,9 +615,20 @@
     int bx = f % 12, by = (f / 12) % 2, z = f / 24;
     int cfg = (z >= 6) ? 1 : 0;
     int kz = cfg ? z - 6 : z;
-    sgemm_body(smem, threadIdx.x,
-               cfg ? Gi : Gt, cfg ? isp_w : tsp_w, cfg ? isn_g : tsn_g,
-               nullptr, nullptr, nullptr, 0, state_tmp, kz, bx, by, D_, D_);
+    float acc[4][4] = {};
+    sgemm_acc_body(smem, threadIdx.x,
+                   cfg ? Gi : Gt, cfg ? isp_w : tsp_w, cfg ? isn_g : tsn_g,
+                   nullptr, nullptr, 0, acc, bx, by, kz * 128, kz * 128 + 128, D_, D_);
+    int tx = threadIdx.x & 15, ty = threadIdx.x >> 4;
+    #pragma unroll
+    for (int i = 0; i < 4; ++i) {
+        int r = by * 64 + ty + 16 * i;
+        #pragma unroll
+        for (int j = 0; j < 4; ++j) {
+            int c = bx * 64 + tx + 16 * j;
+            atomicAdd(&state_tmp[(size_t)r * D_ + c], acc[i][j]);
+        }
+    }
 }
 
 __global__ __launch_bounds__(256) void final_ln_kernel(
@@ -707,7 +723,6 @@
     size_t o = 0;
     float* stats_mu = ws + o; o += 6272;
     float* stats_rs = ws + o; o += 6272;
-    float* zeroBase = ws + o;
     float* b_su_t = ws + o; o += E_;
     float* b_su_i = ws + o; o += E_;
     float* b_tp_t = ws + o; o += E_;
@@ -721,11 +736,8 @@
     float* state_tmp = ws + o; o += (size_t)B_ * K_ * D_;
     float* rs_t = ws + o; o += 128;
     float* rs_i = ws + o; o += 128;
-    size_t zeroFloats = (size_t)(4 * E_ + 2 * D_ + 4 * B_ * K_ * E_ + B_ * K_ * D_ + 256);
     float* Etmp_t = ws + o; o += (size_t)B_ * K_ * ST_;
     float* Etmp_i = ws + o; o += (size_t)B_ * K_ * SI_;
-    ushort_t* AF_t = (ushort_t*)(ws + o); o += (size_t)B_ * ST_ * D_ / 2;
-    ushort_t* AF_i = (ushort_t*)(ws + o); o += (size_t)B_ * SI_ * D_ / 2;
     ushort_t* WsuF_t = (ushort_t*)(ws + o); o += (size_t)D_ * E_ / 2;
     ushort_t* WsuF_i = (ushort_t*)(ws + o); o += (size_t)D_ * E_ / 2;
     ushort_t* sF_t = (ushort_t*)(ws + o); o += (size_t)B_ * ST_ * E_ / 2;
@@ -736,8 +748,6 @@
     ushort_t* XhF_i = (ushort_t*)(ws + o); o += (size_t)B_ * SI_ * D_ / 2;
     ushort_t* XrF_t = (ushort_t*)(ws + o); o += (size_t)B_ * ST_ * D_ / 2;
     ushort_t* XrF_i = (ushort_t*)(ws + o); o += (size_t)B_ * SI_ * D_ / 2;
-    ushort_t* EF_t  = (ushort_t*)(ws + o); o += (size_t)B_ * ST_ * K_ / 2;
-    ushort_t* EF_i  = (ushort_t*)(ws + o); o += (size_t)B_ * SI_ * K_ / 2;
     const int BKD = B_ * K_ * D_;
     float* PtG = ws + o; o += (size_t)16 * BKD;
     float* PtR = ws + o; o += (size_t)16 * BKD;
@@ -752,9 +762,7 @@
     float* t2l = (float*)d_out + 2 * (size_t)B_ * K_ * D_;
     float* i2l = t2l + (size_t)B_ * ST_ * K_;
 
-    hipMemsetAsync(zeroBase, 0, zeroFloats * sizeof(float), stream);
-
-    prelude_kernel<<<2624, 256, 1024, stream>>>(
+    prelude_kernel<<<1785, 256, 8768, stream>>>(
         text_values, image_values, lvalue_init, stats_mu, stats_rs,
         t_sn_b, t_su_w, t_su_b, b_su_t,
         i_sn_b, i_su_w, i_su_b, b_su_i,
@@ -763,33 +771,30 @@
         tsn_b, tsp_w, tsp_b, b_tspf,
         isn_b, isp_w, isp_b, b_ispf,
         t_su_w, t_sn_g, WsuF_t,
-        i_su_w, i_sn_g, WsuF_i);
-
-    stage2_kernel<<<1248, 256, 17152, stream>>>(
+        i_su_w, i_sn_g, WsuF_i,
+        t_tp_w, t_tn_g, b_tp_t, t_t,
+        i_tp_w, i_tn_g, b_tp_i, t_i,
+        rs_t, rs_i);
+
+    bigpack_kernel<<<9552, 256, 18432, stream>>>(
+        t_t, t_i, t_m1_w, t_m1_b, i_m1_w, i_m1_b, c2_t, c2_i,
         text_values, image_values, stats_mu, stats_rs,
-        XrF_t, XhF_t, AF_t, XrF_i, XhF_i, AF_i,
-        lvalue_init,
-        t_tp_w, t_tn_g, b_tp_t, t_t,
-        i_tp_w, i_tn_g, b_tp_i, t_i);
-
-    stage3_kernel<<<8416, 256, 18432, stream>>>(
-        t_t, t_i, t_m1_w, t_m1_b, i_m1_w, i_m1_b, c2_t, c2_i,
-        AF_t, WsuF_t, b_su_t, sF_t,
-        AF_i, WsuF_i, b_su_i, sF_i,
+        WsuF_t, b_su_t, sF_t,
+        WsuF_i, b_su_i, sF_i,
+        XrF_t, XhF_t, XrF_i, XhF_i,
         MF_t, MF_i);
 
     cross_mfma_kernel<<<dim3(K_, 48, B_), 256, 0, stream>>>(
         sF_t, MF_t, c2_t, t_m2_w, t_m2_b, text_mask, Etmp_t,
         sF_i, MF_i, c2_i, i_m2_w, i_m2_b, image_mask, Etmp_i);
 
-    packE2_kernel<<<192, 256, 0, stream>>>(
-        Etmp_t, Etmp_i, t2l, i2l, EF_t, EF_i, rs_t, rs_i);
-
     einsum_mfma_kernel<<<dim3(6, 16, 4), 256, 0, stream>>>(
-        EF_t, XhF_t, XrF_t, PtG, PtR,
-        EF_i, XhF_i, XrF_i, PiG, PiR);
-
-    reduce_parts_kernel<<<(BKD + 255) / 256, 256, 0, stream>>>(PtG, PtR, PiG, PiR, Gt, Gi, Racc);
+        Etmp_t, XhF_t, XrF_t, PtG, PtR,
+        Etmp_i, XhF_i, XrF_i, PiG, PiR,
+        t2l, i2l, rs_t, rs_i);
+
+    reduce_parts_kernel<<<(BKD + 255) / 256, 256, 0, stream>>>(
+        PtG, PtR, PiG, PiR, Gt, Gi, Racc, state_tmp);
 
     sgemm3_kernel<<<288, 256, 8256, stream>>>(
         Gt, tsp_w, tsn_g, Gi, isp_w, isn_g, state_tmp);
```

New measurement: 391.5 us. 1.19x slower.
